# Kernel optimization log

Hardware: AMD Instinct MI355X
Metric: run time of the kernel (lower is better)

Reference implementation:

```python
import jax, jax.numpy as jnp
import numpy as np

EMBED_DIM = 1024
NUM_HEADS = 16
HEAD_DIM = EMBED_DIM // NUM_HEADS


def setup_inputs() -> dict:
    key = jax.random.key(0)
    k_x, k_qw, k_qb, k_ow, k_ob = jax.random.split(key, 5)
    C = EMBED_DIM
    # torch nn.Linear init scale ~ U(-1/sqrt(fan_in), 1/sqrt(fan_in)); use small normals
    s = 1.0 / np.sqrt(C)
    return {
        "x": jax.random.normal(k_x, (4, 2048, C), dtype=jnp.float32),
        "qkv_w": jax.random.uniform(k_qw, (3 * C, C), jnp.float32, -s, s),
        "qkv_b": jax.random.uniform(k_qb, (3 * C,), jnp.float32, -s, s),
        "fc_w": jax.random.uniform(k_ow, (C, C), jnp.float32, -s, s),
        "fc_b": jax.random.uniform(k_ob, (C,), jnp.float32, -s, s),
    }


def reference(x, qkv_w, qkv_b, fc_w, fc_b):
    B, N, C = x.shape
    H, D = NUM_HEADS, HEAD_DIM
    scale = D ** -0.5
    qkv = x @ qkv_w.T + qkv_b                      # [B,N,3C]
    qkv = qkv.reshape(B, N, 3, H, D)
    q, k, v = [jnp.transpose(qkv[:, :, i], (0, 2, 1, 3)) for i in range(3)]  # [B,H,N,D]
    attn = jnp.einsum("bhqd,bhkd->bhqk", q, k) * scale
    attn = jax.nn.softmax(attn, axis=-1)
    out = jnp.einsum("bhqk,bhkd->bhqd", attn, v)   # [B,H,N,D]
    out = jnp.transpose(out, (0, 2, 1, 3)).reshape(B, N, C)
    return out @ fc_w.T + fc_b
```

## Files before the change

kernel.cpp:

```cpp
#include <hip/hip_runtime.h>

#define NUM_HEADS 16
#define HEAD_DIM  64
#define EMB       1024
#define SEQ       2048
#define BATCH     4
#define MROWS     (BATCH * SEQ)
#define QKV_ELEMS (MROWS * EMB)

typedef __attribute__((ext_vector_type(4)))  float  floatx4;
typedef __attribute__((ext_vector_type(16))) float  floatx16;
typedef __attribute__((ext_vector_type(8)))  __bf16 bf16x8;

__device__ __forceinline__ unsigned short f2bf(float f) {
    unsigned int u = __float_as_uint(f);
    u += 0x7fffu + ((u >> 16) & 1u);
    return (unsigned short)(u >> 16);
}

__device__ __forceinline__ ushort4 pk4(float4 v) {
    return make_ushort4(f2bf(v.x), f2bf(v.y), f2bf(v.z), f2bf(v.w));
}

__device__ __forceinline__ uint2 packbf4t(float a0, float a1, float a2, float a3) {
    uint2 r;
    r.x = __builtin_amdgcn_perm(__float_as_uint(a1), __float_as_uint(a0), 0x07060302u);
    r.y = __builtin_amdgcn_perm(__float_as_uint(a3), __float_as_uint(a2), 0x07060302u);
    return r;
}

__device__ __forceinline__ bf16x8 mk8(uint2 lo, uint2 hi) {
    union { uint4 u; bf16x8 b; } cvt;
    cvt.u = make_uint4(lo.x, lo.y, hi.x, hi.y);
    return cvt.b;
}

__device__ __forceinline__ float truncbf(float f) {
    return __uint_as_float(__float_as_uint(f) & 0xffff0000u);
}

#define MFMA16(a, b, c) __builtin_amdgcn_mfma_f32_16x16x32_bf16((a), (b), (c), 0, 0, 0)
#define MFMA32(a, b, c) __builtin_amdgcn_mfma_f32_32x32x16_bf16((a), (b), (c), 0, 0, 0)
#define EXP2(x) __builtin_amdgcn_exp2f(x)

#define BAR() asm volatile("s_barrier" ::: "memory")

__device__ __forceinline__ void async16(const unsigned short* g, unsigned short* l) {
    __builtin_amdgcn_global_load_lds((const __attribute__((address_space(1))) void*)g,
                                     (__attribute__((address_space(3))) void*)l,
                                     16, 0, 0);
}


#define QSCALE 0.18033688011112042f

#define XV4  2097152
#define QWV4 786432
#define FWV4 262144

__global__ __launch_bounds__(256)
void convert_kernel(const float* __restrict__ x, const float* __restrict__ qw,
                    const float* __restrict__ fw,
                    unsigned short* __restrict__ xb, unsigned short* __restrict__ qwb,
                    unsigned short* __restrict__ fwb)
{
    const size_t i = (size_t)blockIdx.x * 256 + threadIdx.x;
    const float* src; unsigned short* dst; size_t off;
    if (i < XV4)              { src = x;  dst = xb;  off = i; }
    else if (i < XV4 + QWV4)  { src = qw; dst = qwb; off = i - XV4; }
    else                      { src = fw; dst = fwb; off = i - (XV4 + QWV4); }
    float4 v = ((const float4*)src)[off];
    ((ushort4*)dst)[off] = pk4(v);
}

__global__ __launch_bounds__(256, 3)
void qkv_kernel(const unsigned short* __restrict__ X, const unsigned short* __restrict__ W,
                const float* __restrict__ BIAS,
                unsigned short* __restrict__ qb, unsigned short* __restrict__ kb,
                unsigned short* __restrict__ vtb)
{
    __shared__ unsigned short As[128 * 32];
    __shared__ unsigned short Bs[128 * 32];

    const int t    = threadIdx.x;
    const int n0   = blockIdx.x * 128;
    const int m0   = blockIdx.y * 128;
    const int wave = t >> 6, lane = t & 63;
    const int wm   = wave & 1, wn = wave >> 1;
    const int l15  = lane & 15, quad = lane >> 4;

    const int srow = wave * 32 + (lane >> 2);
    const int scol = (lane & 3) * 8;
    const int gcol = (((lane & 3) - ((lane >> 3) & 3)) & 3) * 8;
    const unsigned short* gA = X + (size_t)(m0 + srow) * EMB + gcol;
    const unsigned short* gB = W + (size_t)(n0 + srow) * EMB + gcol;
    unsigned short* lA = &As[srow * 32 + scol];
    unsigned short* lB = &Bs[srow * 32 + scol];

    const int arot = (l15 >> 1) & 3;

    const floatx4 zero4 = {0.f, 0.f, 0.f, 0.f};
    floatx4 acc[4][4];
    #pragma unroll
    for (int i = 0; i < 4; ++i)
        #pragma unroll
        for (int j = 0; j < 4; ++j) acc[i][j] = zero4;

    for (int k0 = 0; k0 < EMB; k0 += 32) {
        __syncthreads();
        async16(gA + k0,                     lA);
        async16(gA + k0 + (size_t)16 * EMB,  lA + 16 * 32);
        async16(gB + k0,                     lB);
        async16(gB + k0 + (size_t)16 * EMB,  lB + 16 * 32);
        __syncthreads();

        bf16x8 af[4], bfv[4];
        #pragma unroll
        for (int i = 0; i < 4; ++i) {
            const int pc = ((quad + arot) & 3) * 8;
            af[i]  = *(const bf16x8*)&As[(wm * 64 + i * 16 + l15) * 32 + pc];
            bfv[i] = *(const bf16x8*)&Bs[(wn * 64 + i * 16 + l15) * 32 + pc];
        }
        #pragma unroll
        for (int mi = 0; mi < 4; ++mi)
            #pragma unroll
            for (int ni = 0; ni < 4; ++ni)
                acc[mi][ni] = MFMA16(af[mi], bfv[ni], acc[mi][ni]);
    }

    const int bb = m0 >> 11;
    #pragma unroll
    for (int ni = 0; ni < 4; ++ni) {
        const int gc     = n0 + wn * 64 + ni * 16 + l15;
        const float bias = BIAS[gc];
        const int which  = gc >> 10;
        const int rem    = gc & 1023;
        const int hh     = rem >> 6;
        const int dd     = rem & 63;
        #pragma unroll
        for (int mi = 0; mi < 4; ++mi) {
            const int nseq0 = (m0 & 2047) + wm * 64 + mi * 16 + quad * 4;
            floatx4 v = acc[mi][ni];
            if (which == 2) {
                ushort4 pk;
                pk.x = f2bf(v[0] + bias); pk.y = f2bf(v[1] + bias);
                pk.z = f2bf(v[2] + bias); pk.w = f2bf(v[3] + bias);
                *(ushort4*)&vtb[((size_t)(bb * NUM_HEADS + hh) * HEAD_DIM + dd) * SEQ + nseq0] = pk;
            } else {
                unsigned short* dst = which ? kb : qb;
                const float sc = which ? 1.0f : QSCALE;
                #pragma unroll
                for (int r = 0; r < 4; ++r)
                    dst[((size_t)(bb * NUM_HEADS + hh) * SEQ + (nseq0 + r)) * HEAD_DIM + dd] =
                        f2bf((v[r] + bias) * sc);
            }
        }
    }
}

__global__ __launch_bounds__(512, 4)
void attn_kernel(const unsigned short* __restrict__ qb, const unsigned short* __restrict__ kb,
                 const unsigned short* __restrict__ vtb, unsigned short* __restrict__ attnb)
{
    __shared__ unsigned short smem[2][16384];

    const int t    = threadIdx.x;
    const int bh   = blockIdx.x;
    const int q0   = blockIdx.y * 256;
    const int b    = bh >> 4, hh = bh & 15;
    const int wave = t >> 6, lane = t & 63;
    const int l31  = lane & 31, hl = lane >> 5;
    const int srow = lane >> 2;
    const int scol = (lane & 3) * 8;
    const int gcol = (((lane & 3) - ((lane >> 3) & 3)) & 3) * 8;
    const int rrot = (l31 >> 1) & 3;

    const unsigned short* qp = qb  + (size_t)bh * SEQ * HEAD_DIM;
    const unsigned short* kp = kb  + (size_t)bh * SEQ * HEAD_DIM;
    const unsigned short* vp = vtb + (size_t)bh * HEAD_DIM * SEQ;

    auto stage_kv = [&](int kv0n, unsigned short* B) {
        const int kr = wave * 16 + srow;
        async16(kp + (size_t)(kv0n + kr) * 64 + gcol,      &B[kr * 32 + scol]);
        async16(kp + (size_t)(kv0n + kr) * 64 + 32 + gcol, &B[4096 + kr * 32 + scol]);
        const int kk = wave >> 1;
        #pragma unroll
        for (int j = 0; j < 2; ++j) {
            const int vd = (wave & 1) * 32 + j * 16 + srow;
            async16(vp + (size_t)vd * SEQ + kv0n + kk * 32 + gcol,
                    &B[8192 + kk * 2048 + vd * 32 + scol]);
        }
    };

    {
        const int qr = wave * 16 + srow;
        #pragma unroll
        for (int s = 0; s < 2; ++s)
            #pragma unroll
            for (int h = 0; h < 2; ++h)
                async16(qp + (size_t)(q0 + s * 128 + qr) * 64 + h * 32 + gcol,
                        &smem[1][s * 8192 + h * 4096 + qr * 32 + scol]);
        stage_kv(0, smem[0]);
    }
    asm volatile("s_waitcnt vmcnt(4)" ::: "memory");
    BAR();
    bf16x8 qf[4];
    #pragma unroll
    for (int ks = 0; ks < 4; ++ks)
        qf[ks] = *(const bf16x8*)&smem[1][(wave >> 2) * 8192 + (ks >> 1) * 4096 +
                 ((wave & 3) * 32 + l31) * 32 + ((((ks & 1) * 2 + hl) + rrot) & 3) * 8];
    asm volatile("s_waitcnt lgkmcnt(0)" ::: "memory");
    BAR();

    floatx16 o[2];
    #pragma unroll
    for (int i = 0; i < 16; ++i) { o[0][i] = 0.f; o[1][i] = 0.f; }
    float dsum = 0.f;

    for (int it = 0; it < 16; ++it) {
        const int cur = it & 1;
        if (it < 15) {
            stage_kv((it + 1) * 128, (unsigned short*)smem[cur ^ 1]);
            asm volatile("s_waitcnt vmcnt(4)" ::: "memory");
        } else {
            asm volatile("s_waitcnt vmcnt(0)" ::: "memory");
        }
        BAR();

        const unsigned short* S = smem[cur];

        #pragma unroll
        for (int tt = 0; tt < 4; ++tt) {
            floatx16 st;
            #pragma unroll
            for (int i = 0; i < 16; ++i) st[i] = 0.f;
            __builtin_amdgcn_s_setprio(1);
            #pragma unroll
            for (int ks = 0; ks < 4; ++ks) {
                bf16x8 kf = *(const bf16x8*)&S[(ks >> 1) * 4096 +
                            (tt * 32 + l31) * 32 + ((((ks & 1) * 2 + hl) + rrot) & 3) * 8];
                st = MFMA32(kf, qf[ks], st);
            }
            __builtin_amdgcn_s_setprio(0);

            float ev[16];
            #pragma unroll
            for (int i = 0; i < 16; ++i) ev[i] = EXP2(st[i]);

            {
                float t0  = truncbf(ev[0]),  t1  = truncbf(ev[1]);
                float t2  = truncbf(ev[2]),  t3  = truncbf(ev[3]);
                float t4  = truncbf(ev[4]),  t5  = truncbf(ev[5]);
                float t6  = truncbf(ev[6]),  t7  = truncbf(ev[7]);
                float t8  = truncbf(ev[8]),  t9  = truncbf(ev[9]);
                float t10 = truncbf(ev[10]), t11 = truncbf(ev[11]);
                float t12 = truncbf(ev[12]), t13 = truncbf(ev[13]);
                float t14 = truncbf(ev[14]), t15 = truncbf(ev[15]);
                dsum += (((t0 + t1) + (t2 + t3)) + ((t4 + t5) + (t6 + t7))) +
                        (((t8 + t9) + (t10 + t11)) + ((t12 + t13) + (t14 + t15)));
            }

            uint2 pk0 = packbf4t(ev[0],  ev[1],  ev[2],  ev[3]);
            uint2 pk1 = packbf4t(ev[4],  ev[5],  ev[6],  ev[7]);
            uint2 pk2 = packbf4t(ev[8],  ev[9],  ev[10], ev[11]);
            uint2 pk3 = packbf4t(ev[12], ev[13], ev[14], ev[15]);

            auto sA0 = __builtin_amdgcn_permlane32_swap(pk0.x, pk1.x, false, false);
            auto sA1 = __builtin_amdgcn_permlane32_swap(pk0.y, pk1.y, false, false);
            auto sB0 = __builtin_amdgcn_permlane32_swap(pk2.x, pk3.x, false, false);
            auto sB1 = __builtin_amdgcn_permlane32_swap(pk2.y, pk3.y, false, false);
            bf16x8 pfA = mk8(make_uint2(sA0[0], sA1[0]), make_uint2(sA0[1], sA1[1]));
            bf16x8 pfB = mk8(make_uint2(sB0[0], sB1[0]), make_uint2(sB0[1], sB1[1]));

            __builtin_amdgcn_s_setprio(1);
            #pragma unroll
            for (int s = 0; s < 2; ++s) {
                const bf16x8 pf = s ? pfB : pfA;
                const int kvblk = tt * 2 + s;
                const int vbase = 8192 + (kvblk >> 1) * 2048;
                const int vchun = ((((kvblk & 1) * 2 + hl) + rrot) & 3) * 8;
                #pragma unroll
                for (int dt = 0; dt < 2; ++dt) {
                    bf16x8 vf = *(const bf16x8*)&S[vbase + (dt * 32 + l31) * 32 + vchun];
                    o[dt] = MFMA32(pf, vf, o[dt]);
                }
            }
            __builtin_amdgcn_s_setprio(0);
        }

        asm volatile("s_waitcnt lgkmcnt(0)" ::: "memory");
        BAR();
    }

    float dtot = dsum + __shfl_xor(dsum, 32);

    #pragma unroll
    for (int g = 0; g < 4; ++g)
        #pragma unroll
        for (int e = 0; e < 4; ++e) {
            const float da  = __shfl(dtot, g * 8 + e);
            const float db  = __shfl(dtot, g * 8 + e + 4);
            const float inv = 1.0f / (hl ? db : da);
            const int  qrow = q0 + wave * 32 + e + g * 8 + hl * 4;
            #pragma unroll
            for (int dt = 0; dt < 2; ++dt)
                attnb[(size_t)(b * SEQ + qrow) * EMB + hh * HEAD_DIM + dt * 32 + l31] =
                    f2bf(o[dt][g * 4 + e] * inv);
        }
}

__global__ __launch_bounds__(256, 3)
void proj_kernel(const unsigned short* __restrict__ A, const unsigned short* __restrict__ W,
                 const float* __restrict__ BIAS, float* __restrict__ out)
{
    __shared__ unsigned short As[128 * 32];
    __shared__ unsigned short Bs[128 * 32];

    const int t    = threadIdx.x;
    const int n0   = blockIdx.x * 128;
    const int m0   = blockIdx.y * 128;
    const int wave = t >> 6, lane = t & 63;
    const int wm   = wave & 1, wn = wave >> 1;
    const int l15  = lane & 15, quad = lane >> 4;

    const int srow = wave * 32 + (lane >> 2);
    const int scol = (lane & 3) * 8;
    const int gcol = (((lane & 3) - ((lane >> 3) & 3)) & 3) * 8;
    const unsigned short* gA = A + (size_t)(m0 + srow) * EMB + gcol;
    const unsigned short* gB = W + (size_t)(n0 + srow) * EMB + gcol;
    unsigned short* lA = &As[srow * 32 + scol];
    unsigned short* lB = &Bs[srow * 32 + scol];

    const int arot = (l15 >> 1) & 3;

    const floatx4 zero4 = {0.f, 0.f, 0.f, 0.f};
    floatx4 acc[4][4];
    #pragma unroll
    for (int i = 0; i < 4; ++i)
        #pragma unroll
        for (int j = 0; j < 4; ++j) acc[i][j] = zero4;

    for (int k0 = 0; k0 < EMB; k0 += 32) {
        __syncthreads();
        async16(gA + k0,                     lA);
        async16(gA + k0 + (size_t)16 * EMB,  lA + 16 * 32);
        async16(gB + k0,                     lB);
        async16(gB + k0 + (size_t)16 * EMB,  lB + 16 * 32);
        __syncthreads();

        bf16x8 af[4], bfv[4];
        #pragma unroll
        for (int i = 0; i < 4; ++i) {
            const int pc = ((quad + arot) & 3) * 8;
            af[i]  = *(const bf16x8*)&As[(wm * 64 + i * 16 + l15) * 32 + pc];
            bfv[i] = *(const bf16x8*)&Bs[(wn * 64 + i * 16 + l15) * 32 + pc];
        }
        #pragma unroll
        for (int mi = 0; mi < 4; ++mi)
            #pragma unroll
            for (int ni = 0; ni < 4; ++ni)
                acc[mi][ni] = MFMA16(af[mi], bfv[ni], acc[mi][ni]);
    }

    #pragma unroll
    for (int ni = 0; ni < 4; ++ni) {
        const int gc     = n0 + wn * 64 + ni * 16 + l15;
        const float bias = BIAS[gc];
        #pragma unroll
        for (int mi = 0; mi < 4; ++mi) {
            const int gm = m0 + wm * 64 + mi * 16 + quad * 4;
            #pragma unroll
            for (int r = 0; r < 4; ++r)
                out[(size_t)(gm + r) * EMB + gc] = acc[mi][ni][r] + bias;
        }
    }
}

extern "C" void kernel_launch(void* const* d_in, const int* in_sizes, int n_in,
                              void* d_out, int out_size, void* d_ws, size_t ws_size,
                              hipStream_t stream) {
    (void)in_sizes; (void)n_in; (void)out_size; (void)ws_size;
    const float* x     = (const float*)d_in[0];
    const float* qkv_w = (const float*)d_in[1];
    const float* qkv_b = (const float*)d_in[2];
    const float* fc_w  = (const float*)d_in[3];
    const float* fc_b  = (const float*)d_in[4];
    float* out = (float*)d_out;

    unsigned short* xb    = (unsigned short*)d_ws;
    unsigned short* attnb = xb;
    unsigned short* qbuf  = xb    + QKV_ELEMS;
    unsigned short* kbuf  = qbuf  + QKV_ELEMS;
    unsigned short* vtbuf = kbuf  + QKV_ELEMS;
    unsigned short* qwb   = vtbuf + QKV_ELEMS;
    unsigned short* fwb   = qwb   + 3 * EMB * EMB;

    convert_kernel<<<dim3((XV4 + QWV4 + FWV4) / 256), 256, 0, stream>>>(
        x, qkv_w, fc_w, xb, qwb, fwb);
    qkv_kernel<<<dim3(24, 64), 256, 0, stream>>>(xb, qwb, qkv_b, qbuf, kbuf, vtbuf);
    attn_kernel<<<dim3(64, 8), 512, 0, stream>>>(qbuf, kbuf, vtbuf, attnb);
    proj_kernel<<<dim3(8, 64), 256, 0, stream>>>(attnb, fwb, fc_b, out);
}
```

Baseline: 263.8 us.

## Double-buffer LDS tiles in QKV and projection GEMMs to overlap loads with MFMA

Both GEMM kernels now keep two LDS buffers and issue the async global-to-LDS copies for the next K-slice before computing on the current one. Explicit vmcnt waits and barriers replace the two full __syncthreads per iteration. The aim is to hide global load latency behind the MFMA work. It doubles LDS use per block, to 32 KB, which may reduce occupancy under the 3-blocks-per-CU launch bound. It also depends on the async copy counting correctly under vmcnt.

```diff
diff --git a/kernel.cpp b/kernel.cpp
--- a/kernel.cpp
+++ b/kernel.cpp
@@ -79,8 +79,8 @@
                 unsigned short* __restrict__ qb, unsigned short* __restrict__ kb,
                 unsigned short* __restrict__ vtb)
 {
-    __shared__ unsigned short As[128 * 32];
-    __shared__ unsigned short Bs[128 * 32];
+    __shared__ unsigned short As[2][128 * 32];
+    __shared__ unsigned short Bs[2][128 * 32];
 
     const int t    = threadIdx.x;
     const int n0   = blockIdx.x * 128;
@@ -94,38 +94,51 @@
     const int gcol = (((lane & 3) - ((lane >> 3) & 3)) & 3) * 8;
     const unsigned short* gA = X + (size_t)(m0 + srow) * EMB + gcol;
     const unsigned short* gB = W + (size_t)(n0 + srow) * EMB + gcol;
-    unsigned short* lA = &As[srow * 32 + scol];
-    unsigned short* lB = &Bs[srow * 32 + scol];
 
     const int arot = (l15 >> 1) & 3;
-
-    const floatx4 zero4 = {0.f, 0.f, 0.f, 0.f};
-    floatx4 acc[4][4];
-    #pragma unroll
-    for (int i = 0; i < 4; ++i)
-        #pragma unroll
-        for (int j = 0; j < 4; ++j) acc[i][j] = zero4;
-
-    for (int k0 = 0; k0 < EMB; k0 += 32) {
-        __syncthreads();
+    const int pc   = ((quad + arot) & 3) * 8;
+
+    auto stage = [&](int k0, int buf) {
+        unsigned short* lA = &As[buf][srow * 32 + scol];
+        unsigned short* lB = &Bs[buf][srow * 32 + scol];
         async16(gA + k0,                     lA);
         async16(gA + k0 + (size_t)16 * EMB,  lA + 16 * 32);
         async16(gB + k0,                     lB);
         async16(gB + k0 + (size_t)16 * EMB,  lB + 16 * 32);
-        __syncthreads();
+    };
+
+    const floatx4 zero4 = {0.f, 0.f, 0.f, 0.f};
+    floatx4 acc[4][4];
+    #pragma unroll
+    for (int i = 0; i < 4; ++i)
+        #pragma unroll
+        for (int j = 0; j < 4; ++j) acc[i][j] = zero4;
+
+    stage(0, 0);
+    for (int it = 0; it < 32; ++it) {
+        const int cur = it & 1;
+        if (it < 31) {
+            stage((it + 1) * 32, cur ^ 1);
+            asm volatile("s_waitcnt vmcnt(4)" ::: "memory");
+        } else {
+            asm volatile("s_waitcnt vmcnt(0)" ::: "memory");
+        }
+        BAR();
 
         bf16x8 af[4], bfv[4];
         #pragma unroll
         for (int i = 0; i < 4; ++i) {
-            const int pc = ((quad + arot) & 3) * 8;
-            af[i]  = *(const bf16x8*)&As[(wm * 64 + i * 16 + l15) * 32 + pc];
-            bfv[i] = *(const bf16x8*)&Bs[(wn * 64 + i * 16 + l15) * 32 + pc];
+            af[i]  = *(const bf16x8*)&As[cur][(wm * 64 + i * 16 + l15) * 32 + pc];
+            bfv[i] = *(const bf16x8*)&Bs[cur][(wn * 64 + i * 16 + l15) * 32 + pc];
         }
         #pragma unroll
         for (int mi = 0; mi < 4; ++mi)
             #pragma unroll
             for (int ni = 0; ni < 4; ++ni)
                 acc[mi][ni] = MFMA16(af[mi], bfv[ni], acc[mi][ni]);
+
+        asm volatile("s_waitcnt lgkmcnt(0)" ::: "memory");
+        BAR();
     }
 
     const int bb = m0 >> 11;
@@ -313,8 +326,8 @@
 void proj_kernel(const unsigned short* __restrict__ A, const unsigned short* __restrict__ W,
                  const float* __restrict__ BIAS, float* __restrict__ out)
 {
-    __shared__ unsigned short As[128 * 32];
-    __shared__ unsigned short Bs[128 * 32];
+    __shared__ unsigned short As[2][128 * 32];
+    __shared__ unsigned short Bs[2][128 * 32];
 
     const int t    = threadIdx.x;
     const int n0   = blockIdx.x * 128;
@@ -328,38 +341,51 @@
     const int gcol = (((lane & 3) - ((lane >> 3) & 3)) & 3) * 8;
     const unsigned short* gA = A + (size_t)(m0 + srow) * EMB + gcol;
     const unsigned short* gB = W + (size_t)(n0 + srow) * EMB + gcol;
-    unsigned short* lA = &As[srow * 32 + scol];
-    unsigned short* lB = &Bs[srow * 32 + scol];
 
     const int arot = (l15 >> 1) & 3;
-
-    const floatx4 zero4 = {0.f, 0.f, 0.f, 0.f};
-    floatx4 acc[4][4];
-    #pragma unroll
-    for (int i = 0; i < 4; ++i)
-        #pragma unroll
-        for (int j = 0; j < 4; ++j) acc[i][j] = zero4;
-
-    for (int k0 = 0; k0 < EMB; k0 += 32) {
-        __syncthreads();
+    const int pc   = ((quad + arot) & 3) * 8;
+
+    auto stage = [&](int k0, int buf) {
+        unsigned short* lA = &As[buf][srow * 32 + scol];
+        unsigned short* lB = &Bs[buf][srow * 32 + scol];
         async16(gA + k0,                     lA);
         async16(gA + k0 + (size_t)16 * EMB,  lA + 16 * 32);
         async16(gB + k0,                     lB);
         async16(gB + k0 + (size_t)16 * EMB,  lB + 16 * 32);
-        __syncthreads();
+    };
+
+    const floatx4 zero4 = {0.f, 0.f, 0.f, 0.f};
+    floatx4 acc[4][4];
+    #pragma unroll
+    for (int i = 0; i < 4; ++i)
+        #pragma unroll
+        for (int j = 0; j < 4; ++j) acc[i][j] = zero4;
+
+    stage(0, 0);
+    for (int it = 0; it < 32; ++it) {
+        const int cur = it & 1;
+        if (it < 31) {
+            stage((it + 1) * 32, cur ^ 1);
+            asm volatile("s_waitcnt vmcnt(4)" ::: "memory");
+        } else {
+            asm volatile("s_waitcnt vmcnt(0)" ::: "memory");
+        }
+        BAR();
 
         bf16x8 af[4], bfv[4];
         #pragma unroll
         for (int i = 0; i < 4; ++i) {
-            const int pc = ((quad + arot) & 3) * 8;
-            af[i]  = *(const bf16x8*)&As[(wm * 64 + i * 16 + l15) * 32 + pc];
-            bfv[i] = *(const bf16x8*)&Bs[(wn * 64 + i * 16 + l15) * 32 + pc];
+            af[i]  = *(const bf16x8*)&As[cur][(wm * 64 + i * 16 + l15) * 32 + pc];
+            bfv[i] = *(const bf16x8*)&Bs[cur][(wn * 64 + i * 16 + l15) * 32 + pc];
         }
         #pragma unroll
         for (int mi = 0; mi < 4; ++mi)
             #pragma unroll
             for (int ni = 0; ni < 4; ++ni)
                 acc[mi][ni] = MFMA16(af[mi], bfv[ni], acc[mi][ni]);
+
+        asm volatile("s_waitcnt lgkmcnt(0)" ::: "memory");
+        BAR();
     }
 
     #pragma unroll
```

Result: slower. 271.1 us (+2.7%).

## Enlarge QKV GEMM tiles to 256x256 with double-buffered async LDS prefetch

Applied to the files above, without the earlier changes.

The QKV projection GEMM now uses 256x256 output tiles per 512-thread block, with each wave computing a 128x64 sub-tile. K-slices are double-buffered in LDS, and the next slice is prefetched asynchronously, interleaved between MFMA groups, with priority raised around the MFMAs. The aim is to raise arithmetic intensity per global load and to hide load latency behind compute. The cost is more registers and LDS per block, which lowers occupancy, and a grid of only 384 blocks, which may fill the GPU's CUs unevenly.

```diff
diff --git a/kernel.cpp b/kernel.cpp
--- a/kernel.cpp
+++ b/kernel.cpp
@@ -73,59 +73,83 @@
     ((ushort4*)dst)[off] = pk4(v);
 }
 
-__global__ __launch_bounds__(256, 3)
+__global__ __launch_bounds__(512, 2)
 void qkv_kernel(const unsigned short* __restrict__ X, const unsigned short* __restrict__ W,
                 const float* __restrict__ BIAS,
                 unsigned short* __restrict__ qb, unsigned short* __restrict__ kb,
                 unsigned short* __restrict__ vtb)
 {
-    __shared__ unsigned short As[128 * 32];
-    __shared__ unsigned short Bs[128 * 32];
+    __shared__ unsigned short As[2][256 * 32];
+    __shared__ unsigned short Bs[2][256 * 32];
 
     const int t    = threadIdx.x;
-    const int n0   = blockIdx.x * 128;
-    const int m0   = blockIdx.y * 128;
+    const int n0   = blockIdx.x * 256;
+    const int m0   = blockIdx.y * 256;
     const int wave = t >> 6, lane = t & 63;
     const int wm   = wave & 1, wn = wave >> 1;
     const int l15  = lane & 15, quad = lane >> 4;
 
-    const int srow = wave * 32 + (lane >> 2);
-    const int scol = (lane & 3) * 8;
-    const int gcol = (((lane & 3) - ((lane >> 3) & 3)) & 3) * 8;
+    const int srow = t >> 2;
+    const int scol = (t & 3) * 8;
+    const int gcol = (((t & 3) - ((t >> 3) & 3)) & 3) * 8;
     const unsigned short* gA = X + (size_t)(m0 + srow) * EMB + gcol;
     const unsigned short* gB = W + (size_t)(n0 + srow) * EMB + gcol;
-    unsigned short* lA = &As[srow * 32 + scol];
-    unsigned short* lB = &Bs[srow * 32 + scol];
 
     const int arot = (l15 >> 1) & 3;
+    const int pc   = ((quad + arot) & 3) * 8;
 
     const floatx4 zero4 = {0.f, 0.f, 0.f, 0.f};
-    floatx4 acc[4][4];
-    #pragma unroll
-    for (int i = 0; i < 4; ++i)
+    floatx4 acc[8][4];
+    #pragma unroll
+    for (int i = 0; i < 8; ++i)
         #pragma unroll
         for (int j = 0; j < 4; ++j) acc[i][j] = zero4;
 
-    for (int k0 = 0; k0 < EMB; k0 += 32) {
-        __syncthreads();
-        async16(gA + k0,                     lA);
-        async16(gA + k0 + (size_t)16 * EMB,  lA + 16 * 32);
-        async16(gB + k0,                     lB);
-        async16(gB + k0 + (size_t)16 * EMB,  lB + 16 * 32);
-        __syncthreads();
-
-        bf16x8 af[4], bfv[4];
-        #pragma unroll
-        for (int i = 0; i < 4; ++i) {
-            const int pc = ((quad + arot) & 3) * 8;
-            af[i]  = *(const bf16x8*)&As[(wm * 64 + i * 16 + l15) * 32 + pc];
-            bfv[i] = *(const bf16x8*)&Bs[(wn * 64 + i * 16 + l15) * 32 + pc];
-        }
-        #pragma unroll
-        for (int mi = 0; mi < 4; ++mi)
-            #pragma unroll
-            for (int ni = 0; ni < 4; ++ni)
-                acc[mi][ni] = MFMA16(af[mi], bfv[ni], acc[mi][ni]);
+    async16(gA, &As[0][srow * 32 + scol]);
+    async16(gA + (size_t)128 * EMB, &As[0][(srow + 128) * 32 + scol]);
+    async16(gB, &Bs[0][srow * 32 + scol]);
+    async16(gB + (size_t)128 * EMB, &Bs[0][(srow + 128) * 32 + scol]);
+
+    for (int it = 0; it < 32; ++it) {
+        const int cur = it & 1;
+        const int nxt = cur ^ 1;
+        const int nk  = (it + 1) * 32;
+        const bool pf = it < 31;
+
+        asm volatile("s_waitcnt vmcnt(0)" ::: "memory");
+        BAR();
+
+        const unsigned short* Ab = As[cur];
+        const unsigned short* Bb = Bs[cur];
+
+        bf16x8 bfv[4];
+        #pragma unroll
+        for (int i = 0; i < 4; ++i)
+            bfv[i] = *(const bf16x8*)&Bb[(wn * 64 + i * 16 + l15) * 32 + pc];
+
+        #pragma unroll
+        for (int p = 0; p < 4; ++p) {
+            bf16x8 a0 = *(const bf16x8*)&Ab[(wm * 128 + (2 * p)     * 16 + l15) * 32 + pc];
+            bf16x8 a1 = *(const bf16x8*)&Ab[(wm * 128 + (2 * p + 1) * 16 + l15) * 32 + pc];
+            if (pf) {
+                if      (p == 0) async16(gA + nk,                     &As[nxt][srow * 32 + scol]);
+                else if (p == 1) async16(gA + nk + (size_t)128 * EMB, &As[nxt][(srow + 128) * 32 + scol]);
+                else if (p == 2) async16(gB + nk,                     &Bs[nxt][srow * 32 + scol]);
+                else             async16(gB + nk + (size_t)128 * EMB, &Bs[nxt][(srow + 128) * 32 + scol]);
+            }
+            BAR();
+            __builtin_amdgcn_s_setprio(1);
+            #pragma unroll
+            for (int ni = 0; ni < 4; ++ni) {
+                acc[2 * p][ni]     = MFMA16(a0, bfv[ni], acc[2 * p][ni]);
+                acc[2 * p + 1][ni] = MFMA16(a1, bfv[ni], acc[2 * p + 1][ni]);
+            }
+            __builtin_amdgcn_s_setprio(0);
+            if (p < 3) BAR();
+        }
+
+        asm volatile("s_waitcnt lgkmcnt(0)" ::: "memory");
+        BAR();
     }
 
     const int bb = m0 >> 11;
@@ -138,8 +162,8 @@
         const int hh     = rem >> 6;
         const int dd     = rem & 63;
         #pragma unroll
-        for (int mi = 0; mi < 4; ++mi) {
-            const int nseq0 = (m0 & 2047) + wm * 64 + mi * 16 + quad * 4;
+        for (int mi = 0; mi < 8; ++mi) {
+            const int nseq0 = (m0 & 2047) + wm * 128 + mi * 16 + quad * 4;
             floatx4 v = acc[mi][ni];
             if (which == 2) {
                 ushort4 pk;
@@ -397,7 +421,7 @@
 
     convert_kernel<<<dim3((XV4 + QWV4 + FWV4) / 256), 256, 0, stream>>>(
         x, qkv_w, fc_w, xb, qwb, fwb);
-    qkv_kernel<<<dim3(24, 64), 256, 0, stream>>>(xb, qwb, qkv_b, qbuf, kbuf, vtbuf);
+    qkv_kernel<<<dim3(12, 32), 512, 0, stream>>>(xb, qwb, qkv_b, qbuf, kbuf, vtbuf);
     attn_kernel<<<dim3(64, 8), 512, 0, stream>>>(qbuf, kbuf, vtbuf, attnb);
     proj_kernel<<<dim3(8, 64), 256, 0, stream>>>(attnb, fwb, fc_b, out);
 }
```

Result: slower. 293.8 us (+11.3%).
